# Kernel optimization log

Hardware: AMD Instinct MI355X
Metric: run time of the kernel (lower is better)

Reference implementation:

```python
import jax, jax.numpy as jnp
import numpy as np
import math

B, L, E, H, D = 2, 2048, 2048, 16, 128
LOGIT_SCALE_MAX = math.log(1.0 / 0.01)
EPS = 1e-6


def rms_norm(x, scale, eps=EPS):
    # UIOLayerNorm: no mean subtraction, no bias, fp32 internals
    x32 = x.astype(jnp.float32)
    ms = jnp.mean(x32 * x32, axis=-1, keepdims=True)
    return (scale * (x32 * jax.lax.rsqrt(ms + eps)).astype(x.dtype)).astype(x.dtype)


def apply_rotary(x, rope):
    # x: [b, l, h, d]; rope: [b, l, d] interpreted as (cos, sin) interleaved pairs
    b, l, h, d = x.shape
    xr = x.astype(jnp.float32).reshape(b, l, h, d // 2, 2)
    rc = rope.astype(jnp.float32).reshape(b, l, 1, d // 2, 2)
    out = jnp.stack(
        [xr[..., 0] * rc[..., 0] - xr[..., 1] * rc[..., 1],
         xr[..., 1] * rc[..., 0] + xr[..., 0] * rc[..., 1]], axis=-1)
    return out.reshape(b, l, h, d).astype(x.dtype)


def l2_normalize(x, eps=1e-12):
    # matches F.normalize(dim=-1): x / max(||x||, eps)
    n = jnp.sqrt(jnp.sum(x * x, axis=-1, keepdims=True))
    return x / jnp.maximum(n, eps)


def setup_inputs() -> dict:
    key = jax.random.key(0)
    ks = jax.random.split(key, 12)
    scale = 1.0 / math.sqrt(E)
    return {
        "inputs_q": jax.random.normal(ks[0], (B, L, E), jnp.float32),
        "inputs_kv": jax.random.normal(ks[1], (B, L, E), jnp.float32),
        "bias": jax.random.normal(ks[2], (1, 1, L, L), jnp.float32),
        "q_sinusoids": jax.random.uniform(ks[3], (B, L, D), jnp.float32, -1.0, 1.0),
        "k_sinusoids": jax.random.uniform(ks[4], (B, L, D), jnp.float32, -1.0, 1.0),
        "Wq": jax.random.normal(ks[5], (E, E), jnp.float32) * scale,
        "Wk": jax.random.normal(ks[6], (E, E), jnp.float32) * scale,
        "Wv": jax.random.normal(ks[7], (E, E), jnp.float32) * scale,
        "Wo": jax.random.normal(ks[8], (E, E), jnp.float32) * scale,
        "q_norm_scale": jnp.ones((D,), jnp.float32),
        "k_norm_scale": jnp.ones((D,), jnp.float32),
        "logit_scale": jnp.full((H,), math.log(10.0), jnp.float32),
    }


def reference(inputs_q, inputs_kv, bias, q_sinusoids, k_sinusoids,
              Wq, Wk, Wv, Wo, q_norm_scale, k_norm_scale, logit_scale):
    dtype = inputs_q.dtype
    b, ql, e = inputs_q.shape
    kl = inputs_kv.shape[1]
    # QKV projections (nn.Linear, no bias), split heads -> [b, len, h, d]
    q = (inputs_q @ Wq.T).reshape(b, ql, H, D)
    k = (inputs_kv @ Wk.T).reshape(b, kl, H, D)
    v = (inputs_kv @ Wv.T).reshape(b, kl, H, D)
    # qk_norm (UIO RMS norm over head_dim)
    q = rms_norm(q, q_norm_scale)
    k = rms_norm(k, k_norm_scale)
    # RoPE
    q = apply_rotary(q, q_sinusoids)
    k = apply_rotary(k, k_sinusoids)
    # float32_logits
    q32 = q.astype(jnp.float32)
    k32 = k.astype(jnp.float32)
    # scaled cosine attention: L2-normalize q,k; learned per-head logit scale
    scores = jnp.einsum("bqhd,bkhd->bhqk", l2_normalize(q32), l2_normalize(k32))
    ls = jnp.exp(jnp.minimum(logit_scale, LOGIT_SCALE_MAX))
    scores = scores * ls[None, :, None, None]
    scores = scores + bias.astype(scores.dtype)
    attn = jax.nn.softmax(scores, axis=-1).astype(dtype)
    out = jnp.einsum("bhqk,bkhd->bqhd", attn, v)
    out = out.reshape(b, ql, e)
    return out @ Wo.T
```

## Files before the change

### kernel.cpp

```cpp
#include <hip/hip_runtime.h>
#include <hip/hip_bf16.h>

#define B_ 2
#define L_ 2048
#define E_ 2048
#define H_ 16
#define D_ 128
#define M_ (B_*L_)
#define NT_ (E_/64)
#define LOGIT_SCALE_MAX_ 4.6051701859880914f
#define LOG2E_ 1.44269504088896f

typedef __bf16 bf16_t;
typedef __bf16 bf16x2 __attribute__((ext_vector_type(2)));
typedef __bf16 bf16x4 __attribute__((ext_vector_type(4)));
typedef __bf16 bf16x8 __attribute__((ext_vector_type(8)));
typedef float f32x4 __attribute__((ext_vector_type(4)));
typedef float f32x16 __attribute__((ext_vector_type(16)));

#define KSB(p, r, cb) ((p) * 32768 + (r) * 256 + ((cb) ^ (((r) & 7) << 4)))
#define VSB(p, r, cb) ((p) * 32768 + 16384 + (r) * 128 + ((cb) ^ (((r) & 7) << 4)))

#define GEMM_FRAG_IDX(r, kk, fq) ((r) * 64 + ((((kk) * 4 + (fq)) ^ ((r) & 7)) * 8))

#define NW_ 4194304L
#define NX_ 8388608L
__global__ void cvt_all_k(const float* __restrict__ xq, const float* __restrict__ xkv,
                          const float* __restrict__ bias,
                          const float* __restrict__ wq, const float* __restrict__ wk,
                          const float* __restrict__ wv, const float* __restrict__ wo,
                          bf16_t* __restrict__ ws) {
    const long NW4 = NW_ / 4, NX4 = NX_ / 4;
    long i4 = (long)blockIdx.x * 256 + threadIdx.x;
    const float* src; long off; float scale = 1.0f;
    if (i4 < 4 * NW4) {
        long r = i4 / NW4;
        src = (r == 0) ? wq : (r == 1) ? wk : (r == 2) ? wv : wo;
        off = i4 - r * NW4;
    } else if (i4 < 5 * NW4) {
        src = bias; off = i4 - 4 * NW4; scale = LOG2E_;
    } else if (i4 < 5 * NW4 + NX4) {
        src = xq; off = i4 - 5 * NW4;
    } else {
        src = xkv; off = i4 - 5 * NW4 - NX4;
    }
    float4 v = ((const float4*)src)[off];
    bf16x4 o = { (bf16_t)(v.x * scale), (bf16_t)(v.y * scale),
                 (bf16_t)(v.z * scale), (bf16_t)(v.w * scale) };
    ((bf16x4*)ws)[i4] = o;
}

template<typename OutT, int GROUPS>
__global__ __launch_bounds__(256, 2) void gemm_pipe(
    const bf16_t* __restrict__ A0, const bf16_t* __restrict__ A1,
    const bf16_t* __restrict__ W0, OutT* __restrict__ C0) {
    __shared__ bf16_t As[2][128 * 64];
    __shared__ bf16_t Bs[2][128 * 64];
    const int tid = threadIdx.x;
    const int wid = tid >> 6, lane = tid & 63;
    int bid = blockIdx.x;
    {
        int cpx = (int)gridDim.x >> 3;
        bid = (bid & 7) * cpx + (bid >> 3);
    }
    const int g = bid >> 9;
    const int wg = bid & 511;
    const int bm = wg >> 4, bn = wg & 15;
    const long arow0 = (long)bm * 128;
    const long brow0 = (long)bn * 128;
    const int fr = lane & 15, fq = lane >> 4;
    const int srow = lane >> 3;
    const int scol = ((lane & 7) ^ srow) * 8;
    const int wm = wid >> 1, wn = wid & 1;
    const bf16_t* Ab = ((GROUPS > 1 && g > 0) ? A1 : A0) + arow0 * E_;
    const bf16_t* Wb = W0 + (long)g * E_ * E_ + brow0 * E_;
    OutT* Cg = C0 + (long)g * M_ * E_;

    f32x4 acc[4][4] = {};

    auto STAGE = [&](int kt, int p) {
        #pragma unroll
        for (int q = 0; q < 4; ++q) {
            int row = wid * 32 + q * 8 + srow;
            __builtin_amdgcn_global_load_lds(
                (const __attribute__((address_space(1))) void*)(Ab + (long)row * E_ + kt + scol),
                (__attribute__((address_space(3))) void*)(&As[p][(wid * 32 + q * 8) * 64]), 16, 0, 0);
            __builtin_amdgcn_global_load_lds(
                (const __attribute__((address_space(1))) void*)(Wb + (long)row * E_ + kt + scol),
                (__attribute__((address_space(3))) void*)(&Bs[p][(wid * 32 + q * 8) * 64]), 16, 0, 0);
        }
    };

    STAGE(0, 0);
    int p = 0;
    bf16x8 a[2][4], b[2][4];
    for (int t = 0; t < NT_ - 1; ++t) {
        STAGE((t + 1) * 64, p ^ 1);
        asm volatile("s_waitcnt vmcnt(8)" ::: "memory");
        __builtin_amdgcn_s_barrier();
        __builtin_amdgcn_sched_barrier(0);
        #pragma unroll
        for (int kk = 0; kk < 2; ++kk) {
            #pragma unroll
            for (int mi = 0; mi < 4; ++mi)
                a[kk][mi] = *(const bf16x8*)&As[p][GEMM_FRAG_IDX(wm * 64 + mi * 16 + fr, kk, fq)];
            #pragma unroll
            for (int ni = 0; ni < 4; ++ni)
                b[kk][ni] = *(const bf16x8*)&Bs[p][GEMM_FRAG_IDX(wn * 64 + ni * 16 + fr, kk, fq)];
        }
        asm volatile("s_waitcnt lgkmcnt(0)" ::: "memory");
        __builtin_amdgcn_sched_barrier(0);
        __builtin_amdgcn_s_barrier();
        __builtin_amdgcn_s_setprio(1);
        #pragma unroll
        for (int kk = 0; kk < 2; ++kk)
            #pragma unroll
            for (int mi = 0; mi < 4; ++mi)
                #pragma unroll
                for (int ni = 0; ni < 4; ++ni)
                    acc[mi][ni] = __builtin_amdgcn_mfma_f32_16x16x32_bf16(a[kk][mi], b[kk][ni], acc[mi][ni], 0, 0, 0);
        __builtin_amdgcn_s_setprio(0);
        p ^= 1;
    }
    asm volatile("s_waitcnt vmcnt(0)" ::: "memory");
    __builtin_amdgcn_s_barrier();
    __builtin_amdgcn_sched_barrier(0);
    #pragma unroll
    for (int kk = 0; kk < 2; ++kk) {
        #pragma unroll
        for (int mi = 0; mi < 4; ++mi)
            a[kk][mi] = *(const bf16x8*)&As[p][GEMM_FRAG_IDX(wm * 64 + mi * 16 + fr, kk, fq)];
        #pragma unroll
        for (int ni = 0; ni < 4; ++ni)
            b[kk][ni] = *(const bf16x8*)&Bs[p][GEMM_FRAG_IDX(wn * 64 + ni * 16 + fr, kk, fq)];
        #pragma unroll
        for (int mi = 0; mi < 4; ++mi)
            #pragma unroll
            for (int ni = 0; ni < 4; ++ni)
                acc[mi][ni] = __builtin_amdgcn_mfma_f32_16x16x32_bf16(a[kk][mi], b[kk][ni], acc[mi][ni], 0, 0, 0);
    }
    #pragma unroll
    for (int mi = 0; mi < 4; ++mi) {
        #pragma unroll
        for (int i = 0; i < 4; ++i) {
            long row = arow0 + wm * 64 + mi * 16 + fq * 4 + i;
            OutT* crow = Cg + row * E_ + brow0 + wn * 64 + fr;
            #pragma unroll
            for (int ni = 0; ni < 4; ++ni)
                crow[ni * 16] = (OutT)acc[mi][ni][i];
        }
    }
}

__global__ __launch_bounds__(256) void post_tv_k(
    const bf16_t* __restrict__ Pq, const bf16_t* __restrict__ Pk,
    const bf16_t* __restrict__ Vp,
    const float* __restrict__ qsins, const float* __restrict__ ksins,
    const float* __restrict__ qnscale, const float* __restrict__ knscale,
    bf16_t* __restrict__ outq, bf16_t* __restrict__ outk, bf16_t* __restrict__ Vt) {
    __shared__ bf16_t t[64 * 64];
    if (blockIdx.x < 32768) {
        const int wid = threadIdx.x >> 6, lane = threadIdx.x & 63;
        const int half = blockIdx.x >> 14;
        const long g = (long)(blockIdx.x & 16383) * 4 + wid;
        const bf16_t* P = half ? Pk : Pq;
        const float* sins = half ? ksins : qsins;
        const float* nscale = half ? knscale : qnscale;
        bf16_t* out = half ? outk : outq;
        const int h = (int)(g % H_);
        const long bl = g / H_;
        const int b = (int)(bl / L_), l = (int)(bl % L_);
        bf16x2 xv = *(const bf16x2*)(P + g * D_ + lane * 2);
        float x0 = (float)xv[0], x1 = (float)xv[1];
        float ss = x0 * x0 + x1 * x1;
        #pragma unroll
        for (int m = 1; m < 64; m <<= 1) ss += __shfl_xor(ss, m);
        float r = rsqrtf(ss * (1.0f / 128.0f) + 1e-6f);
        float y0 = x0 * r * nscale[lane * 2];
        float y1 = x1 * r * nscale[lane * 2 + 1];
        float2 cs = *(const float2*)(sins + bl * D_ + lane * 2);
        float z0 = y0 * cs.x - y1 * cs.y;
        float z1 = y1 * cs.x + y0 * cs.y;
        float n2 = z0 * z0 + z1 * z1;
        #pragma unroll
        for (int m = 1; m < 64; m <<= 1) n2 += __shfl_xor(n2, m);
        float inv = 1.0f / fmaxf(sqrtf(n2), 1e-12f);
        bf16x2 o = { (bf16_t)(z0 * inv), (bf16_t)(z1 * inv) };
        *(bf16x2*)(out + (((long)b * H_ + h) * L_ + l) * D_ + lane * 2) = o;
    } else {
        const int idx = blockIdx.x - 32768;
        const int lb = idx & 31;
        const int db = (idx >> 5) & 1;
        const int bh = idx >> 6;
        const int b = bh >> 4, h = bh & 15;
        const bf16_t* src = Vp + ((long)(b * L_ + lb * 64) * H_ + h) * D_ + db * 64;
        #pragma unroll
        for (int it = 0; it < 2; ++it) {
            int i = it * 256 + threadIdx.x;
            int r = i >> 3, c8 = i & 7;
            bf16x8 v = *(const bf16x8*)(src + (long)r * H_ * D_ + c8 * 8);
            *(bf16x8*)&t[r * 64 + (c8 ^ (r >> 3)) * 8] = v;
        }
        __syncthreads();
        bf16_t* dst = Vt + ((long)(b * H_ + h) * D_ + db * 64) * L_ + lb * 64;
        #pragma unroll
        for (int it = 0; it < 2; ++it) {
            int i = it * 256 + threadIdx.x;
            int d = i >> 3, l8 = i & 7;
            bf16x8 o;
            #pragma unroll
            for (int j = 0; j < 8; ++j) {
                int l = l8 * 8 + j;
                o[j] = t[l * 64 + ((d >> 3) ^ l8) * 8 + (d & 7)];
            }
            *(bf16x8*)(dst + (long)d * L_ + l8 * 8) = o;
        }
    }
}

__global__ __launch_bounds__(256, 2) void attn_k(
    const bf16_t* __restrict__ Qn, const bf16_t* __restrict__ Kn,
    const bf16_t* __restrict__ Vt, const bf16_t* __restrict__ biasb,
    const float* __restrict__ lsg, bf16_t* __restrict__ AO) {
    __shared__ __align__(16) unsigned char smem[65536];
    const int tid = threadIdx.x;
    const int w = tid >> 6, lane = tid & 63;
    const int lane31 = lane & 31, hi = lane >> 5;
    const int qb = blockIdx.x, bh = blockIdx.y;
    const int b = bh >> 4, h = bh & 15;
    const float lsc2 = __expf(fminf(lsg[h], LOGIT_SCALE_MAX_)) * LOG2E_;
    const int qr0 = qb * 128;
    const int qloc = w * 32 + lane31;
    const bf16_t* qrow  = Qn + (((long)b * H_ + h) * L_ + qr0 + qloc) * D_;
    const bf16_t* kbase = Kn + (((long)b * H_ + h) * L_) * D_;
    const bf16_t* vtbase = Vt + ((long)(b * H_ + h) * D_) * L_;
    const bf16_t* brow  = biasb + (long)(qr0 + qloc) * L_;

    const int ksr = tid >> 4, ksc = (tid & 15) * 8;
    const int vsr = tid >> 3, vsc = (tid & 7) * 8;

    bf16x8 qreg[8];
    #pragma unroll
    for (int kk = 0; kk < 8; ++kk)
        qreg[kk] = *(const bf16x8*)(qrow + kk * 16 + 8 * hi);

    f32x16 oacc[4] = {};
    float l_ = 0.f;

    bf16x8 kreg[4], vreg[4];
    #pragma unroll
    for (int it = 0; it < 4; ++it) {
        kreg[it] = *(const bf16x8*)(kbase + (long)(it * 16 + ksr) * D_ + ksc);
        vreg[it] = *(const bf16x8*)(vtbase + (long)(it * 32 + vsr) * L_ + vsc);
    }
    #pragma unroll
    for (int it = 0; it < 4; ++it) {
        *(bf16x8*)(smem + KSB(0, it * 16 + ksr, ksc * 2)) = kreg[it];
        *(bf16x8*)(smem + VSB(0, it * 32 + vsr, vsc * 2)) = vreg[it];
    }
    int p = 0;

    for (int kt = 0; kt < L_; kt += 64) {
        __syncthreads();
        const int ktn = (kt + 64 < L_) ? kt + 64 : 0;
        #pragma unroll
        for (int it = 0; it < 4; ++it) {
            kreg[it] = *(const bf16x8*)(kbase + (long)(ktn + it * 16 + ksr) * D_ + ksc);
            vreg[it] = *(const bf16x8*)(vtbase + (long)(it * 32 + vsr) * L_ + ktn + vsc);
        }
        bf16x4 bb[2][4];
        #pragma unroll
        for (int f = 0; f < 2; ++f)
            #pragma unroll
            for (int rr = 0; rr < 4; ++rr)
                bb[f][rr] = *(const bf16x4*)(brow + kt + f * 32 + rr * 8 + 4 * hi);
        f32x16 sacc[2] = {};
        __builtin_amdgcn_s_setprio(1);
        #pragma unroll
        for (int kk = 0; kk < 8; ++kk) {
            bf16x8 ak0 = *(const bf16x8*)(smem + KSB(p, lane31,      kk * 32 + 16 * hi));
            bf16x8 ak1 = *(const bf16x8*)(smem + KSB(p, 32 + lane31, kk * 32 + 16 * hi));
            sacc[0] = __builtin_amdgcn_mfma_f32_32x32x16_bf16(ak0, qreg[kk], sacc[0], 0, 0, 0);
            sacc[1] = __builtin_amdgcn_mfma_f32_32x32x16_bf16(ak1, qreg[kk], sacc[1], 0, 0, 0);
        }
        __builtin_amdgcn_s_setprio(0);
        float ps = 0.f;
        unsigned int wv[2][4][2];
        #pragma unroll
        for (int f = 0; f < 2; ++f)
            #pragma unroll
            for (int rr = 0; rr < 4; ++rr)
                #pragma unroll
                for (int wi = 0; wi < 2; ++wi) {
                    float pa = __builtin_amdgcn_exp2f(sacc[f][rr * 4 + wi * 2]     * lsc2 + (float)bb[f][rr][wi * 2]);
                    float pc = __builtin_amdgcn_exp2f(sacc[f][rr * 4 + wi * 2 + 1] * lsc2 + (float)bb[f][rr][wi * 2 + 1]);
                    ps += pa + pc;
                    bf16x2 t = { (bf16_t)pa, (bf16_t)pc };
                    wv[f][rr][wi] = __builtin_bit_cast(unsigned int, t);
                }
        ps += __shfl_xor(ps, 32);
        l_ += ps;
        bf16x8 pb_[4];
        #pragma unroll
        for (int kk = 0; kk < 4; ++kk) {
            const int f = kk >> 1;
            const int a2 = (kk & 1) * 2;
            unsigned int A0 = wv[f][a2][0],     A1 = wv[f][a2][1];
            unsigned int B0 = wv[f][a2 + 1][0], B1 = wv[f][a2 + 1][1];
            unsigned int own0  = hi ? B0 : A0;
            unsigned int own1  = hi ? B1 : A1;
            unsigned int send0 = hi ? A0 : B0;
            unsigned int send1 = hi ? A1 : B1;
            unsigned int recv0 = __shfl_xor(send0, 32);
            unsigned int recv1 = __shfl_xor(send1, 32);
            uint4 uu;
            uu.x = hi ? recv0 : own0;
            uu.y = hi ? recv1 : own1;
            uu.z = hi ? own0  : recv0;
            uu.w = hi ? own1  : recv1;
            pb_[kk] = __builtin_bit_cast(bf16x8, uu);
        }
        __builtin_amdgcn_s_setprio(1);
        #pragma unroll
        for (int df = 0; df < 4; ++df)
            #pragma unroll
            for (int kk = 0; kk < 4; ++kk) {
                bf16x8 av = *(const bf16x8*)(smem + VSB(p, df * 32 + lane31, kk * 32 + 16 * hi));
                oacc[df] = __builtin_amdgcn_mfma_f32_32x32x16_bf16(av, pb_[kk], oacc[df], 0, 0, 0);
            }
        __builtin_amdgcn_s_setprio(0);
        if (kt + 64 < L_) {
            #pragma unroll
            for (int it = 0; it < 4; ++it) {
                *(bf16x8*)(smem + KSB(p ^ 1, it * 16 + ksr, ksc * 2)) = kreg[it];
                *(bf16x8*)(smem + VSB(p ^ 1, it * 32 + vsr, vsc * 2)) = vreg[it];
            }
        }
        p ^= 1;
    }
    __syncthreads();
    float inv = 1.0f / l_;
    #pragma unroll
    for (int df = 0; df < 4; ++df)
        #pragma unroll
        for (int rg = 0; rg < 16; ++rg) {
            int d = df * 32 + (rg & 3) + 8 * (rg >> 2) + 4 * hi;
            *(bf16_t*)(smem + qloc * 264 + d * 2) = (bf16_t)(oacc[df][rg] * inv);
        }
    __syncthreads();
    #pragma unroll
    for (int it = 0; it < 8; ++it) {
        int idx = it * 256 + tid;
        int row = idx >> 4, c = idx & 15;
        bf16x8 v = *(const bf16x8*)(smem + row * 264 + c * 16);
        *(bf16x8*)(AO + ((long)b * L_ + qr0 + row) * E_ + h * D_ + c * 8) = v;
    }
}

extern "C" void kernel_launch(void* const* d_in, const int* in_sizes, int n_in,
                              void* d_out, int out_size, void* d_ws, size_t ws_size,
                              hipStream_t stream) {
    const float* inputs_q  = (const float*)d_in[0];
    const float* inputs_kv = (const float*)d_in[1];
    const float* bias      = (const float*)d_in[2];
    const float* q_sin     = (const float*)d_in[3];
    const float* k_sin     = (const float*)d_in[4];
    const float* Wq        = (const float*)d_in[5];
    const float* Wk        = (const float*)d_in[6];
    const float* Wv        = (const float*)d_in[7];
    const float* Wo        = (const float*)d_in[8];
    const float* qns       = (const float*)d_in[9];
    const float* kns       = (const float*)d_in[10];
    const float* lsg       = (const float*)d_in[11];

    bf16_t* ws = (bf16_t*)d_ws;
    const long NW = NW_;
    const long NX = NX_;
    bf16_t* Wq_b   = ws;
    bf16_t* Wo_b   = ws + 3 * NW;
    bf16_t* bias_b = ws + 4 * NW;
    bf16_t* Xq     = bias_b + NW;
    bf16_t* Xkv    = Xq + NX;
    bf16_t* Qp     = Xkv + NX;
    bf16_t* Kp     = Qp + NX;
    bf16_t* Vp     = Kp + NX;
    bf16_t* Qn = Xq;
    bf16_t* Kn = Xkv;
    bf16_t* AO = Qp;
    bf16_t* Vtr = Kp;
    if (ws_size < (size_t)(5 * NW + 5 * NX) * 2) return;

    {
        long n4 = (5 * NW + 2 * NX) / 4;
        cvt_all_k<<<dim3((unsigned)(n4 / 256)), dim3(256), 0, stream>>>(
            inputs_q, inputs_kv, bias, Wq, Wk, Wv, Wo, ws);
    }

    gemm_pipe<bf16_t, 3><<<dim3(1536), dim3(256), 0, stream>>>(Xq, Xkv, Wq_b, Qp);

    post_tv_k<<<dim3(34816), dim3(256), 0, stream>>>(
        Qp, Kp, Vp, q_sin, k_sin, qns, kns, Qn, Kn, Vtr);

    attn_k<<<dim3(L_ / 128, B_ * H_), dim3(256), 0, stream>>>(Qn, Kn, Vtr, bias_b, lsg, AO);

    gemm_pipe<float, 1><<<dim3(512), dim3(256), 0, stream>>>(AO, AO, Wo_b, (float*)d_out);
}
```

Baseline: 314.5 us.

## Fuse QK norm, RoPE, L2 normalize and V transpose into QKV GEMM epilogue

```diff
diff --git a/kernel.cpp b/kernel.cpp
--- a/kernel.cpp
+++ b/kernel.cpp
@@ -50,10 +50,13 @@
     ((bf16x4*)ws)[i4] = o;
 }
 
-template<typename OutT, int GROUPS>
-__global__ __launch_bounds__(256, 2) void gemm_pipe(
+template<typename OutT, int GROUPS, bool FUSE>
+__global__ __launch_bounds__(256, 4) void gemm_pipe(
     const bf16_t* __restrict__ A0, const bf16_t* __restrict__ A1,
-    const bf16_t* __restrict__ W0, OutT* __restrict__ C0) {
+    const bf16_t* __restrict__ W0, OutT* __restrict__ C0,
+    const float* __restrict__ sq, const float* __restrict__ sk,
+    const float* __restrict__ nq, const float* __restrict__ nk,
+    bf16_t* __restrict__ Qn, bf16_t* __restrict__ Kn, bf16_t* __restrict__ Vt) {
     __shared__ bf16_t As[2][128 * 64];
     __shared__ bf16_t Bs[2][128 * 64];
     const int tid = threadIdx.x;
@@ -74,7 +77,6 @@
     const int wm = wid >> 1, wn = wid & 1;
     const bf16_t* Ab = ((GROUPS > 1 && g > 0) ? A1 : A0) + arow0 * E_;
     const bf16_t* Wb = W0 + (long)g * E_ * E_ + brow0 * E_;
-    OutT* Cg = C0 + (long)g * M_ * E_;
 
     f32x4 acc[4][4] = {};
 
@@ -139,81 +141,89 @@
             for (int ni = 0; ni < 4; ++ni)
                 acc[mi][ni] = __builtin_amdgcn_mfma_f32_16x16x32_bf16(a[kk][mi], b[kk][ni], acc[mi][ni], 0, 0, 0);
     }
-    #pragma unroll
-    for (int mi = 0; mi < 4; ++mi) {
-        #pragma unroll
-        for (int i = 0; i < 4; ++i) {
-            long row = arow0 + wm * 64 + mi * 16 + fq * 4 + i;
-            OutT* crow = Cg + row * E_ + brow0 + wn * 64 + fr;
-            #pragma unroll
-            for (int ni = 0; ni < 4; ++ni)
-                crow[ni * 16] = (OutT)acc[mi][ni][i];
-        }
-    }
-}
-
-__global__ __launch_bounds__(256) void post_tv_k(
-    const bf16_t* __restrict__ Pq, const bf16_t* __restrict__ Pk,
-    const bf16_t* __restrict__ Vp,
-    const float* __restrict__ qsins, const float* __restrict__ ksins,
-    const float* __restrict__ qnscale, const float* __restrict__ knscale,
-    bf16_t* __restrict__ outq, bf16_t* __restrict__ outk, bf16_t* __restrict__ Vt) {
-    __shared__ bf16_t t[64 * 64];
-    if (blockIdx.x < 32768) {
-        const int wid = threadIdx.x >> 6, lane = threadIdx.x & 63;
-        const int half = blockIdx.x >> 14;
-        const long g = (long)(blockIdx.x & 16383) * 4 + wid;
-        const bf16_t* P = half ? Pk : Pq;
-        const float* sins = half ? ksins : qsins;
-        const float* nscale = half ? knscale : qnscale;
-        bf16_t* out = half ? outk : outq;
-        const int h = (int)(g % H_);
-        const long bl = g / H_;
-        const int b = (int)(bl / L_), l = (int)(bl % L_);
-        bf16x2 xv = *(const bf16x2*)(P + g * D_ + lane * 2);
-        float x0 = (float)xv[0], x1 = (float)xv[1];
-        float ss = x0 * x0 + x1 * x1;
-        #pragma unroll
-        for (int m = 1; m < 64; m <<= 1) ss += __shfl_xor(ss, m);
-        float r = rsqrtf(ss * (1.0f / 128.0f) + 1e-6f);
-        float y0 = x0 * r * nscale[lane * 2];
-        float y1 = x1 * r * nscale[lane * 2 + 1];
-        float2 cs = *(const float2*)(sins + bl * D_ + lane * 2);
-        float z0 = y0 * cs.x - y1 * cs.y;
-        float z1 = y1 * cs.x + y0 * cs.y;
-        float n2 = z0 * z0 + z1 * z1;
-        #pragma unroll
-        for (int m = 1; m < 64; m <<= 1) n2 += __shfl_xor(n2, m);
-        float inv = 1.0f / fmaxf(sqrtf(n2), 1e-12f);
-        bf16x2 o = { (bf16_t)(z0 * inv), (bf16_t)(z1 * inv) };
-        *(bf16x2*)(out + (((long)b * H_ + h) * L_ + l) * D_ + lane * 2) = o;
+
+    if constexpr (FUSE) {
+        __syncthreads();
+        float* eps = (float*)&As[0][0];
+        #pragma unroll
+        for (int mi = 0; mi < 4; ++mi)
+            #pragma unroll
+            for (int i = 0; i < 4; ++i) {
+                int rl = wm * 64 + mi * 16 + fq * 4 + i;
+                #pragma unroll
+                for (int ni = 0; ni < 4; ++ni) {
+                    int c = wn * 64 + ni * 16 + fr;
+                    eps[rl * 128 + ((((c >> 2) ^ (rl & 7)) << 2) | (c & 3))] = acc[mi][ni][i];
+                }
+            }
+        __syncthreads();
+        const int r = tid >> 1, hf = tid & 1;
+        if (g < 2) {
+            const float* sins = (g == 0) ? sq : sk;
+            const float* nsc  = (g == 0) ? nq : nk;
+            bf16_t* outb      = (g == 0) ? Qn : Kn;
+            const int rowg = (int)arow0 + r;
+            const int bb2 = rowg >> 11, ll = rowg & 2047;
+            const float* sinrow = sins + (long)rowg * 128 + hf * 64;
+            float ss = 0.f;
+            #pragma unroll
+            for (int c = 0; c < 16; ++c) {
+                float4 v = *(float4*)&eps[r * 128 + (((hf * 16 + c) ^ (r & 7)) << 2)];
+                ss += v.x * v.x + v.y * v.y + v.z * v.z + v.w * v.w;
+            }
+            ss += __shfl_xor(ss, 1);
+            float rms = rsqrtf(ss * (1.f / 128.f) + 1e-6f);
+            float n2 = 0.f;
+            #pragma unroll
+            for (int c = 0; c < 16; ++c) {
+                int ix = r * 128 + (((hf * 16 + c) ^ (r & 7)) << 2);
+                float4 v = *(float4*)&eps[ix];
+                float4 s4 = *(const float4*)&sinrow[c * 4];
+                float4 n4 = *(const float4*)&nsc[hf * 64 + c * 4];
+                float y0 = v.x * rms * n4.x, y1 = v.y * rms * n4.y;
+                float y2 = v.z * rms * n4.z, y3 = v.w * rms * n4.w;
+                float4 z;
+                z.x = y0 * s4.x - y1 * s4.y;  z.y = y1 * s4.x + y0 * s4.y;
+                z.z = y2 * s4.z - y3 * s4.w;  z.w = y3 * s4.z + y2 * s4.w;
+                n2 += z.x * z.x + z.y * z.y + z.z * z.z + z.w * z.w;
+                *(float4*)&eps[ix] = z;
+            }
+            n2 += __shfl_xor(n2, 1);
+            float inv = 1.f / fmaxf(sqrtf(n2), 1e-12f);
+            bf16_t* outp = outb + (((long)bb2 * H_ + bn) * L_ + ll) * D_ + hf * 64;
+            #pragma unroll
+            for (int c2 = 0; c2 < 8; ++c2) {
+                float4 v0 = *(float4*)&eps[r * 128 + (((hf * 16 + c2 * 2)     ^ (r & 7)) << 2)];
+                float4 v1 = *(float4*)&eps[r * 128 + (((hf * 16 + c2 * 2 + 1) ^ (r & 7)) << 2)];
+                bf16x8 o = { (bf16_t)(v0.x * inv), (bf16_t)(v0.y * inv), (bf16_t)(v0.z * inv), (bf16_t)(v0.w * inv),
+                             (bf16_t)(v1.x * inv), (bf16_t)(v1.y * inv), (bf16_t)(v1.z * inv), (bf16_t)(v1.w * inv) };
+                *(bf16x8*)(outp + c2 * 8) = o;
+            }
+        } else {
+            bf16_t* vout = Vt + (((long)(bm >> 4) * H_ + bn) * D_ + r) * L_ + (bm & 15) * 128 + hf * 64;
+            #pragma unroll
+            for (int c8 = 0; c8 < 8; ++c8) {
+                bf16x8 o;
+                #pragma unroll
+                for (int j = 0; j < 8; ++j) {
+                    int l = hf * 64 + c8 * 8 + j;
+                    o[j] = (bf16_t)eps[l * 128 + ((((r >> 2) ^ (l & 7)) << 2) | (r & 3))];
+                }
+                *(bf16x8*)(vout + c8 * 8) = o;
+            }
+        }
     } else {
-        const int idx = blockIdx.x - 32768;
-        const int lb = idx & 31;
-        const int db = (idx >> 5) & 1;
-        const int bh = idx >> 6;
-        const int b = bh >> 4, h = bh & 15;
-        const bf16_t* src = Vp + ((long)(b * L_ + lb * 64) * H_ + h) * D_ + db * 64;
-        #pragma unroll
-        for (int it = 0; it < 2; ++it) {
-            int i = it * 256 + threadIdx.x;
-            int r = i >> 3, c8 = i & 7;
-            bf16x8 v = *(const bf16x8*)(src + (long)r * H_ * D_ + c8 * 8);
-            *(bf16x8*)&t[r * 64 + (c8 ^ (r >> 3)) * 8] = v;
-        }
-        __syncthreads();
-        bf16_t* dst = Vt + ((long)(b * H_ + h) * D_ + db * 64) * L_ + lb * 64;
-        #pragma unroll
-        for (int it = 0; it < 2; ++it) {
-            int i = it * 256 + threadIdx.x;
-            int d = i >> 3, l8 = i & 7;
-            bf16x8 o;
-            #pragma unroll
-            for (int j = 0; j < 8; ++j) {
-                int l = l8 * 8 + j;
-                o[j] = t[l * 64 + ((d >> 3) ^ l8) * 8 + (d & 7)];
-            }
-            *(bf16x8*)(dst + (long)d * L_ + l8 * 8) = o;
+        OutT* Cg = C0 + (long)g * M_ * E_;
+        #pragma unroll
+        for (int mi = 0; mi < 4; ++mi) {
+            #pragma unroll
+            for (int i = 0; i < 4; ++i) {
+                long row = arow0 + wm * 64 + mi * 16 + fq * 4 + i;
+                OutT* crow = Cg + row * E_ + brow0 + wn * 64 + fr;
+                #pragma unroll
+                for (int ni = 0; ni < 4; ++ni)
+                    crow[ni * 16] = (OutT)acc[mi][ni][i];
+            }
         }
     }
 }
@@ -381,13 +391,10 @@
     bf16_t* bias_b = ws + 4 * NW;
     bf16_t* Xq     = bias_b + NW;
     bf16_t* Xkv    = Xq + NX;
-    bf16_t* Qp     = Xkv + NX;
-    bf16_t* Kp     = Qp + NX;
-    bf16_t* Vp     = Kp + NX;
-    bf16_t* Qn = Xq;
-    bf16_t* Kn = Xkv;
-    bf16_t* AO = Qp;
-    bf16_t* Vtr = Kp;
+    bf16_t* Qn     = Xkv + NX;
+    bf16_t* Kn     = Qn + NX;
+    bf16_t* Vtr    = Kn + NX;
+    bf16_t* AO     = Xq;
     if (ws_size < (size_t)(5 * NW + 5 * NX) * 2) return;
 
     {
@@ -396,12 +403,11 @@
             inputs_q, inputs_kv, bias, Wq, Wk, Wv, Wo, ws);
     }
 
-    gemm_pipe<bf16_t, 3><<<dim3(1536), dim3(256), 0, stream>>>(Xq, Xkv, Wq_b, Qp);
-
-    post_tv_k<<<dim3(34816), dim3(256), 0, stream>>>(
-        Qp, Kp, Vp, q_sin, k_sin, qns, kns, Qn, Kn, Vtr);
+    gemm_pipe<bf16_t, 3, true><<<dim3(1536), dim3(256), 0, stream>>>(
+        Xq, Xkv, Wq_b, (bf16_t*)nullptr, q_sin, k_sin, qns, kns, Qn, Kn, Vtr);
 
     attn_k<<<dim3(L_ / 128, B_ * H_), dim3(256), 0, stream>>>(Qn, Kn, Vtr, bias_b, lsg, AO);
 
-    gemm_pipe<float, 1><<<dim3(512), dim3(256), 0, stream>>>(AO, AO, Wo_b, (float*)d_out);
+    gemm_pipe<float, 1, false><<<dim3(512), dim3(256), 0, stream>>>(
+        AO, AO, Wo_b, (float*)d_out, nullptr, nullptr, nullptr, nullptr, nullptr, nullptr, nullptr);
 }
```

New measurement: 344.0 us. 9.4% more time.

## Replace GEMM with 8-wave 256x128 tile kernel using interleaved staging and MFMA phases

Applied to the files above, without the earlier changes.

```diff
diff --git a/kernel.cpp b/kernel.cpp
--- a/kernel.cpp
+++ b/kernel.cpp
@@ -7,7 +7,6 @@
 #define H_ 16
 #define D_ 128
 #define M_ (B_*L_)
-#define NT_ (E_/64)
 #define LOGIT_SCALE_MAX_ 4.6051701859880914f
 #define LOG2E_ 1.44269504088896f
 
@@ -21,10 +20,9 @@
 #define KSB(p, r, cb) ((p) * 32768 + (r) * 256 + ((cb) ^ (((r) & 7) << 4)))
 #define VSB(p, r, cb) ((p) * 32768 + 16384 + (r) * 128 + ((cb) ^ (((r) & 7) << 4)))
 
-#define GEMM_FRAG_IDX(r, kk, fq) ((r) * 64 + ((((kk) * 4 + (fq)) ^ ((r) & 7)) * 8))
-
 #define NW_ 4194304L
 #define NX_ 8388608L
+
 __global__ void cvt_all_k(const float* __restrict__ xq, const float* __restrict__ xkv,
                           const float* __restrict__ bias,
                           const float* __restrict__ wq, const float* __restrict__ wk,
@@ -51,94 +49,120 @@
 }
 
 template<typename OutT, int GROUPS>
-__global__ __launch_bounds__(256, 2) void gemm_pipe(
-    const bf16_t* __restrict__ A0, const bf16_t* __restrict__ A1,
+__global__ __launch_bounds__(512, 2) void gemm8(
+    const bf16_t* __restrict__ A0g, const bf16_t* __restrict__ A1g,
     const bf16_t* __restrict__ W0, OutT* __restrict__ C0) {
-    __shared__ bf16_t As[2][128 * 64];
-    __shared__ bf16_t Bs[2][128 * 64];
+    __shared__ __align__(16) unsigned char smem[98304];
     const int tid = threadIdx.x;
     const int wid = tid >> 6, lane = tid & 63;
+    const int fr = lane & 15, fq = lane >> 4;
+    const int wm = wid & 3, wn = wid >> 2;
     int bid = blockIdx.x;
-    {
-        int cpx = (int)gridDim.x >> 3;
-        bid = (bid & 7) * cpx + (bid >> 3);
-    }
-    const int g = bid >> 9;
-    const int wg = bid & 511;
+    { int cpx = (int)gridDim.x >> 3; bid = (bid & 7) * cpx + (bid >> 3); }
+    const int g = (GROUPS > 1) ? (bid >> 8) : 0;
+    const int wg = bid & 255;
     const int bm = wg >> 4, bn = wg & 15;
-    const long arow0 = (long)bm * 128;
+    const long arow0 = (long)bm * 256;
     const long brow0 = (long)bn * 128;
-    const int fr = lane & 15, fq = lane >> 4;
-    const int srow = lane >> 3;
-    const int scol = ((lane & 7) ^ srow) * 8;
-    const int wm = wid >> 1, wn = wid & 1;
-    const bf16_t* Ab = ((GROUPS > 1 && g > 0) ? A1 : A0) + arow0 * E_;
-    const bf16_t* Wb = W0 + (long)g * E_ * E_ + brow0 * E_;
-    OutT* Cg = C0 + (long)g * M_ * E_;
+    const bf16_t* Ab = ((GROUPS > 1 && g > 0) ? A1g : A0g) + arow0 * E_;
+    const bf16_t* Wb = W0 + (long)g * (long)E_ * E_ + brow0 * E_;
 
     f32x4 acc[4][4] = {};
 
-    auto STAGE = [&](int kt, int p) {
-        #pragma unroll
-        for (int q = 0; q < 4; ++q) {
-            int row = wid * 32 + q * 8 + srow;
-            __builtin_amdgcn_global_load_lds(
-                (const __attribute__((address_space(1))) void*)(Ab + (long)row * E_ + kt + scol),
-                (__attribute__((address_space(3))) void*)(&As[p][(wid * 32 + q * 8) * 64]), 16, 0, 0);
-            __builtin_amdgcn_global_load_lds(
-                (const __attribute__((address_space(1))) void*)(Wb + (long)row * E_ + kt + scol),
-                (__attribute__((address_space(3))) void*)(&Bs[p][(wid * 32 + q * 8) * 64]), 16, 0, 0);
-        }
+    auto STAGE_A = [&](unsigned sbase, int kk, int j, int ktn_) {
+        int row = j * 128 + (tid >> 2);
+        int c16 = tid & 3;
+        int col = kk * 32 + ((c16 ^ ((row >> 1) & 3)) * 8);
+        __builtin_amdgcn_global_load_lds(
+            (const __attribute__((address_space(1))) void*)(Ab + (long)row * E_ + ktn_ + col),
+            (__attribute__((address_space(3))) void*)(smem + sbase + kk * 16384 + j * 8192 + tid * 16), 16, 0, 0);
     };
-
-    STAGE(0, 0);
-    int p = 0;
-    bf16x8 a[2][4], b[2][4];
-    for (int t = 0; t < NT_ - 1; ++t) {
-        STAGE((t + 1) * 64, p ^ 1);
-        asm volatile("s_waitcnt vmcnt(8)" ::: "memory");
-        __builtin_amdgcn_s_barrier();
-        __builtin_amdgcn_sched_barrier(0);
-        #pragma unroll
-        for (int kk = 0; kk < 2; ++kk) {
-            #pragma unroll
-            for (int mi = 0; mi < 4; ++mi)
-                a[kk][mi] = *(const bf16x8*)&As[p][GEMM_FRAG_IDX(wm * 64 + mi * 16 + fr, kk, fq)];
-            #pragma unroll
-            for (int ni = 0; ni < 4; ++ni)
-                b[kk][ni] = *(const bf16x8*)&Bs[p][GEMM_FRAG_IDX(wn * 64 + ni * 16 + fr, kk, fq)];
-        }
+    auto STAGE_B = [&](unsigned sbase, int kk, int ktn_) {
+        int row = tid >> 2;
+        int c16 = tid & 3;
+        int col = kk * 32 + ((c16 ^ ((row >> 1) & 3)) * 8);
+        __builtin_amdgcn_global_load_lds(
+            (const __attribute__((address_space(1))) void*)(Wb + (long)row * E_ + ktn_ + col),
+            (__attribute__((address_space(3))) void*)(smem + sbase + 32768 + kk * 8192 + tid * 16), 16, 0, 0);
+    };
+    auto LDA = [&](unsigned pbase, int kk, int mi) -> bf16x8 {
+        int row = wm * 64 + mi * 16 + fr;
+        return *(const bf16x8*)(smem + pbase + kk * 16384 + row * 64 + ((fq ^ ((row >> 1) & 3)) << 4));
+    };
+    auto LDB = [&](unsigned pbase, int kk, int ni) -> bf16x8 {
+        int row = wn * 64 + ni * 16 + fr;
+        return *(const bf16x8*)(smem + pbase + 32768 + kk * 8192 + row * 64 + ((fq ^ ((row >> 1) & 3)) << 4));
+    };
+
+    STAGE_A(0, 0, 0, 0); STAGE_A(0, 0, 1, 0); STAGE_B(0, 0, 0);
+    STAGE_A(0, 1, 0, 0); STAGE_A(0, 1, 1, 0); STAGE_B(0, 1, 0);
+    asm volatile("s_waitcnt vmcnt(0)" ::: "memory");
+    __builtin_amdgcn_s_barrier();
+
+    #pragma unroll 2
+    for (int t = 0; t < 32; ++t) {
+        const unsigned pb = (unsigned)(t & 1) * 49152u;
+        const unsigned sb = 49152u - pb;
+        const int ktn = (t < 31) ? (t + 1) * 64 : 0;
+        bf16x8 bq[4], a0, a1;
+        a0 = LDA(pb, 0, 0); a1 = LDA(pb, 0, 1);
+        bq[0] = LDB(pb, 0, 0); bq[1] = LDB(pb, 0, 1); bq[2] = LDB(pb, 0, 2); bq[3] = LDB(pb, 0, 3);
+        STAGE_A(sb, 0, 0, ktn); STAGE_A(sb, 0, 1, ktn);
+        __builtin_amdgcn_s_barrier();
         asm volatile("s_waitcnt lgkmcnt(0)" ::: "memory");
         __builtin_amdgcn_sched_barrier(0);
-        __builtin_amdgcn_s_barrier();
-        __builtin_amdgcn_s_setprio(1);
-        #pragma unroll
-        for (int kk = 0; kk < 2; ++kk)
-            #pragma unroll
-            for (int mi = 0; mi < 4; ++mi)
-                #pragma unroll
-                for (int ni = 0; ni < 4; ++ni)
-                    acc[mi][ni] = __builtin_amdgcn_mfma_f32_16x16x32_bf16(a[kk][mi], b[kk][ni], acc[mi][ni], 0, 0, 0);
-        __builtin_amdgcn_s_setprio(0);
-        p ^= 1;
-    }
-    asm volatile("s_waitcnt vmcnt(0)" ::: "memory");
-    __builtin_amdgcn_s_barrier();
-    __builtin_amdgcn_sched_barrier(0);
-    #pragma unroll
-    for (int kk = 0; kk < 2; ++kk) {
-        #pragma unroll
-        for (int mi = 0; mi < 4; ++mi)
-            a[kk][mi] = *(const bf16x8*)&As[p][GEMM_FRAG_IDX(wm * 64 + mi * 16 + fr, kk, fq)];
-        #pragma unroll
-        for (int ni = 0; ni < 4; ++ni)
-            b[kk][ni] = *(const bf16x8*)&Bs[p][GEMM_FRAG_IDX(wn * 64 + ni * 16 + fr, kk, fq)];
-        #pragma unroll
-        for (int mi = 0; mi < 4; ++mi)
-            #pragma unroll
-            for (int ni = 0; ni < 4; ++ni)
-                acc[mi][ni] = __builtin_amdgcn_mfma_f32_16x16x32_bf16(a[kk][mi], b[kk][ni], acc[mi][ni], 0, 0, 0);
-    }
+        __builtin_amdgcn_s_setprio(1);
+        #pragma unroll
+        for (int ni = 0; ni < 4; ++ni) {
+            acc[0][ni] = __builtin_amdgcn_mfma_f32_16x16x32_bf16(a0, bq[ni], acc[0][ni], 0, 0, 0);
+            acc[1][ni] = __builtin_amdgcn_mfma_f32_16x16x32_bf16(a1, bq[ni], acc[1][ni], 0, 0, 0);
+        }
+        __builtin_amdgcn_s_setprio(0);
+        __builtin_amdgcn_s_barrier();
+        a0 = LDA(pb, 0, 2); a1 = LDA(pb, 0, 3);
+        STAGE_B(sb, 0, ktn);
+        asm volatile("s_waitcnt vmcnt(3)" ::: "memory");
+        __builtin_amdgcn_s_barrier();
+        asm volatile("s_waitcnt lgkmcnt(0)" ::: "memory");
+        __builtin_amdgcn_sched_barrier(0);
+        __builtin_amdgcn_s_setprio(1);
+        #pragma unroll
+        for (int ni = 0; ni < 4; ++ni) {
+            acc[2][ni] = __builtin_amdgcn_mfma_f32_16x16x32_bf16(a0, bq[ni], acc[2][ni], 0, 0, 0);
+            acc[3][ni] = __builtin_amdgcn_mfma_f32_16x16x32_bf16(a1, bq[ni], acc[3][ni], 0, 0, 0);
+        }
+        __builtin_amdgcn_s_setprio(0);
+        __builtin_amdgcn_s_barrier();
+        a0 = LDA(pb, 1, 0); a1 = LDA(pb, 1, 1);
+        bq[0] = LDB(pb, 1, 0); bq[1] = LDB(pb, 1, 1); bq[2] = LDB(pb, 1, 2); bq[3] = LDB(pb, 1, 3);
+        STAGE_A(sb, 1, 0, ktn); STAGE_A(sb, 1, 1, ktn);
+        __builtin_amdgcn_s_barrier();
+        asm volatile("s_waitcnt lgkmcnt(0)" ::: "memory");
+        __builtin_amdgcn_sched_barrier(0);
+        __builtin_amdgcn_s_setprio(1);
+        #pragma unroll
+        for (int ni = 0; ni < 4; ++ni) {
+            acc[0][ni] = __builtin_amdgcn_mfma_f32_16x16x32_bf16(a0, bq[ni], acc[0][ni], 0, 0, 0);
+            acc[1][ni] = __builtin_amdgcn_mfma_f32_16x16x32_bf16(a1, bq[ni], acc[1][ni], 0, 0, 0);
+        }
+        __builtin_amdgcn_s_setprio(0);
+        __builtin_amdgcn_s_barrier();
+        a0 = LDA(pb, 1, 2); a1 = LDA(pb, 1, 3);
+        STAGE_B(sb, 1, ktn);
+        asm volatile("s_waitcnt vmcnt(3)" ::: "memory");
+        __builtin_amdgcn_s_barrier();
+        asm volatile("s_waitcnt lgkmcnt(0)" ::: "memory");
+        __builtin_amdgcn_sched_barrier(0);
+        __builtin_amdgcn_s_setprio(1);
+        #pragma unroll
+        for (int ni = 0; ni < 4; ++ni) {
+            acc[2][ni] = __builtin_amdgcn_mfma_f32_16x16x32_bf16(a0, bq[ni], acc[2][ni], 0, 0, 0);
+            acc[3][ni] = __builtin_amdgcn_mfma_f32_16x16x32_bf16(a1, bq[ni], acc[3][ni], 0, 0, 0);
+        }
+        __builtin_amdgcn_s_setprio(0);
+        __builtin_amdgcn_s_barrier();
+    }
+    OutT* Cg = C0 + (long)g * M_ * E_;
     #pragma unroll
     for (int mi = 0; mi < 4; ++mi) {
         #pragma unroll
@@ -396,12 +420,12 @@
             inputs_q, inputs_kv, bias, Wq, Wk, Wv, Wo, ws);
     }
 
-    gemm_pipe<bf16_t, 3><<<dim3(1536), dim3(256), 0, stream>>>(Xq, Xkv, Wq_b, Qp);
+    gemm8<bf16_t, 3><<<dim3(768), dim3(512), 0, stream>>>(Xq, Xkv, Wq_b, Qp);
 
     post_tv_k<<<dim3(34816), dim3(256), 0, stream>>>(
         Qp, Kp, Vp, q_sin, k_sin, qns, kns, Qn, Kn, Vtr);
 
     attn_k<<<dim3(L_ / 128, B_ * H_), dim3(256), 0, stream>>>(Qn, Kn, Vtr, bias_b, lsg, AO);
 
-    gemm_pipe<float, 1><<<dim3(512), dim3(256), 0, stream>>>(AO, AO, Wo_b, (float*)d_out);
+    gemm8<float, 1><<<dim3(256), dim3(512), 0, stream>>>(AO, AO, Wo_b, (float*)d_out);
 }
```

Measured after the change: 320.0 us. Within noise of the previous version (+1.7%).
